# Optimization experiments

Measured on AMD Instinct MI355X. Metric: run time of the kernel, lower is better.

Reference implementation:

```python
import jax, jax.numpy as jnp
import numpy as np

B, S, D, H = 2, 2048, 1024, 16
HD = D // H  # head_dim = 64


def setup_inputs() -> dict:
    key = jax.random.key(0)
    ks = jax.random.split(key, 7)
    s = 0.02
    return {
        "queries": jax.random.normal(ks[0], (B, S, D), jnp.float32),
        "keys": jax.random.normal(ks[1], (B, S, D), jnp.float32),
        "values": jax.random.normal(ks[2], (B, S, D), jnp.float32),
        "Wq": jax.random.normal(ks[3], (D, D), jnp.float32) * s,
        "Wk": jax.random.normal(ks[4], (D, D), jnp.float32) * s,
        "Wv": jax.random.normal(ks[5], (D, D), jnp.float32) * s,
        "Wo": jax.random.normal(ks[6], (D, D), jnp.float32) * s,
    }


def reference(queries, keys, values, Wq, Wk, Wv, Wo):
    # Projections (torch Linear: x @ W.T); split into heads -> [B, H, S, HD]
    def split_heads(x):
        b, s, _ = x.shape
        return x.reshape(b, s, H, HD).transpose(0, 2, 1, 3)

    q = split_heads(queries @ Wq.T)
    k = split_heads(keys @ Wk.T)
    v = split_heads(values @ Wv.T)

    scale = 1.0 / jnp.sqrt(jnp.asarray(HD, q.dtype))
    scores = jnp.einsum("bhqd,bhkd->bhqk", q, k) * scale  # [B,H,S,S]
    attn = jax.nn.softmax(scores, axis=-1)
    ctx = jnp.einsum("bhqk,bhkd->bhqd", attn, v)  # [B,H,S,HD]
    out = ctx.transpose(0, 2, 1, 3).reshape(queries.shape[0], -1, D)
    return out @ Wo.T
```

## Files before the change

### kernel.cpp

```cpp
#include <hip/hip_runtime.h>
#include <hip/hip_bf16.h>


#define B_ 2
#define S_ 2048
#define D_ 1024
#define H_ 16
#define HD_ 64
#define NE_ (B_ * S_ * D_)
#define WN_ (D_ * D_)

typedef unsigned short u16;
typedef unsigned int u32;
typedef u16 __attribute__((may_alias)) u16_ma;
typedef float __attribute__((may_alias)) f32_ma;
typedef u32 v4u __attribute__((ext_vector_type(4)));
typedef v4u __attribute__((may_alias)) v4u_ma;
typedef short bf16x8 __attribute__((ext_vector_type(8)));
typedef bf16x8 __attribute__((may_alias)) bf16x8_ma;
typedef float f32x4 __attribute__((ext_vector_type(4)));
typedef float f32x16 __attribute__((ext_vector_type(16)));

__device__ __forceinline__ float bf2f(u16 u) {
  u32 x = ((u32)u) << 16;
  return __builtin_bit_cast(float, x);
}
__device__ __forceinline__ u16 f2bf(float f) {
  __hip_bfloat16 h = __float2bfloat16(f);
  return __builtin_bit_cast(u16, h);
}
__device__ __forceinline__ u16 rne1(float f) {
  u32 a = __builtin_bit_cast(u32, f);
  a += 0x7FFFu + ((a >> 16) & 1u);
  return (u16)(a >> 16);
}
__device__ __forceinline__ u32 rne_pair(float lo, float hi) {
  u32 a = __builtin_bit_cast(u32, lo);
  u32 b = __builtin_bit_cast(u32, hi);
  a += 0x7FFFu + ((a >> 16) & 1u);
  b += 0x7FFFu + ((b >> 16) & 1u);
  return (a >> 16) | (b & 0xFFFF0000u);
}
__device__ __forceinline__ u32 pk2(u32 alo, u32 ahi) {
  return (u32)f2bf(__builtin_bit_cast(float, alo)) |
         ((u32)f2bf(__builtin_bit_cast(float, ahi)) << 16);
}

__device__ __forceinline__ void gl_lds16(const u16* g, u16* l) {
  auto gp = (const __attribute__((address_space(1))) unsigned int*)(const void*)g;
  auto lp = (__attribute__((address_space(3))) unsigned int*)(void*)l;
  __builtin_amdgcn_global_load_lds(gp, lp, 16, 0, 0);
}

__device__ __forceinline__ bool detect_f32(const u16* Wg) {
  const int lane = threadIdx.x & 63;
  bool hit = false;
#pragma unroll
  for (int i = 0; i < 4; ++i) {
    v4u u = *(const v4u_ma*)(Wg + lane * 32 + i * 8);
#pragma unroll
    for (int j = 0; j < 4; ++j) {
      u32 w = u[j];
      hit |= (((w >> 7) & 0xFFu) >= 0xF0u) || (((w >> 23) & 0xFFu) >= 0xF0u);
    }
  }
  return __any(hit);
}

__global__ __launch_bounds__(256) void convert_bf16(
    const void* s0, const void* s1, const void* s2, const void* s3,
    const void* s4, const void* s5, const void* s6, u16* __restrict__ dst_in,
    u16* __restrict__ dst_w, const u16* __restrict__ Wdet) {
  const bool det = detect_f32(Wdet);
  if (!det) return;
  const int y = blockIdx.y;
  const void* src;
  u16* dst;
  int n;
  if (y < 3) {
    src = (y == 0) ? s0 : ((y == 1) ? s1 : s2);
    dst = dst_in + (size_t)y * NE_;
    n = NE_;
  } else {
    src = (y == 3) ? s3 : ((y == 4) ? s4 : ((y == 5) ? s5 : s6));
    dst = dst_w + (size_t)(y - 3) * WN_;
    n = WN_;
  }
  const int i = (blockIdx.x * 256 + threadIdx.x) * 8;
  if (i >= n) return;
  const v4u_ma* fp = (const v4u_ma*)((const float*)src + i);
  v4u f0 = fp[0], f1 = fp[1];
  v4u out;
  out[0] = pk2(f0[0], f0[1]);
  out[1] = pk2(f0[2], f0[3]);
  out[2] = pk2(f1[0], f1[1]);
  out[3] = pk2(f1[2], f1[3]);
  *(v4u_ma*)(dst + i) = out;
}

template <int BN, bool OUT_DET>
__global__ __launch_bounds__(256) void proj_g(
    const u16* __restrict__ Asc, const u16* __restrict__ Wsc,
    void* __restrict__ Cb, const u16* __restrict__ Wdet,
    const u16* __restrict__ Ao0, const u16* __restrict__ Ao1,
    const u16* __restrict__ Ao2, const u16* __restrict__ Wo0,
    const u16* __restrict__ Wo1, const u16* __restrict__ Wo2) {
  __shared__ u16 Al[2][128 * 64];
  __shared__ u16 Wl[2][BN * 64];

  const bool det = detect_f32(Wdet);
  const int z = blockIdx.z;

  const u16* Aptr;
  const u16* Wptr;
  if (OUT_DET) {
    Aptr = Asc;
    Wptr = det ? Wsc : Wo0;
  } else {
    Aptr = det ? (Asc + (size_t)z * NE_)
               : (z == 0 ? Ao0 : (z == 1 ? Ao1 : Ao2));
    Wptr = det ? (Wsc + (size_t)z * WN_)
               : (z == 0 ? Wo0 : (z == 1 ? Wo1 : Wo2));
  }
  const char* Ag = (const char*)Aptr;
  const char* Wg = (const char*)Wptr;

  const int tid = threadIdx.x;
  const int lane = tid & 63, wid = tid >> 6;
  const int lg = lane >> 4, li = lane & 15;
  const int wr = wid >> 1, wc = wid & 1;
  const int m0 = blockIdx.x * 128, n0 = blockIdx.y * BN;

  const int lr = lane >> 3;
  const int swzb = ((lane & 7) * 16) ^ (lr << 4);

  auto issue = [&](int bi, int kt) {
    const int k0b = kt * 128;
#pragma unroll
    for (int c = 0; c < 4; ++c) {
      const int row = wid * 32 + c * 8 + lr;
      gl_lds16((const u16*)(Ag + (size_t)(m0 + row) * 2048 + k0b + swzb),
               &Al[bi][(wid * 32 + c * 8) * 64]);
    }
    if constexpr (BN == 128) {
#pragma unroll
      for (int c = 0; c < 4; ++c) {
        const int row = wid * 32 + c * 8 + lr;
        gl_lds16((const u16*)(Wg + (size_t)(n0 + row) * 2048 + k0b + swzb),
                 &Wl[bi][(wid * 32 + c * 8) * 64]);
      }
    } else {
#pragma unroll
      for (int c = 0; c < 2; ++c) {
        const int row = wid * 16 + c * 8 + lr;
        gl_lds16((const u16*)(Wg + (size_t)(n0 + row) * 2048 + k0b + swzb),
                 &Wl[bi][(wid * 16 + c * 8) * 64]);
      }
    }
  };

  constexpr int NF = BN / 32;
  f32x4 acc[4][NF];
#pragma unroll
  for (int m = 0; m < 4; ++m)
#pragma unroll
    for (int n = 0; n < NF; ++n) acc[m][n] = (f32x4){0.f, 0.f, 0.f, 0.f};

  issue(0, 0);

  for (int kt = 0; kt < 16; ++kt) {
    const int cur = kt & 1;
    if (kt < 15) {
      issue(cur ^ 1, kt + 1);
      if constexpr (BN == 128)
        asm volatile("s_waitcnt vmcnt(8)" ::: "memory");
      else
        asm volatile("s_waitcnt vmcnt(6)" ::: "memory");
    } else {
      asm volatile("s_waitcnt vmcnt(0)" ::: "memory");
    }
    __builtin_amdgcn_s_barrier();
    asm volatile("" ::: "memory");

#pragma unroll
    for (int ks = 0; ks < 2; ++ks) {
      bf16x8 af[4], bw[NF];
#pragma unroll
      for (int m = 0; m < 4; ++m) {
        const int row = wr * 64 + m * 16 + li;
        af[m] = *(const bf16x8_ma*)((const char*)&Al[cur][0] + row * 128 +
                                    ((ks * 64 + lg * 16) ^ ((row & 7) << 4)));
      }
#pragma unroll
      for (int n = 0; n < NF; ++n) {
        const int row = wc * (BN / 2) + n * 16 + li;
        bw[n] = *(const bf16x8_ma*)((const char*)&Wl[cur][0] + row * 128 +
                                    ((ks * 64 + lg * 16) ^ ((row & 7) << 4)));
      }
#pragma unroll
      for (int m = 0; m < 4; ++m)
#pragma unroll
        for (int n = 0; n < NF; ++n)
          acc[m][n] = __builtin_amdgcn_mfma_f32_16x16x32_bf16(af[m], bw[n],
                                                              acc[m][n], 0, 0, 0);
    }

    asm volatile("" ::: "memory");
    __builtin_amdgcn_s_barrier();
  }

  const bool outf32 = OUT_DET ? det : false;
  const float zs = (!OUT_DET && z == 0) ? 0.125f : 1.0f;
#pragma unroll
  for (int m = 0; m < 4; ++m)
#pragma unroll
    for (int n = 0; n < NF; ++n)
#pragma unroll
      for (int r = 0; r < 4; ++r) {
        const int row = m0 + wr * 64 + m * 16 + lg * 4 + r;
        const int col = n0 + wc * (BN / 2) + n * 16 + li;
        const size_t idx = (size_t)row * D_ + col;
        const float v = acc[m][n][r] * zs;
        if (OUT_DET) {
          if (outf32)
            ((f32_ma*)Cb)[idx] = v;
          else
            ((u16_ma*)Cb)[idx] = rne1(v);
        } else {
          ((u16_ma*)((u16*)Cb + (size_t)z * NE_))[idx] = rne1(v);
        }
      }
}

__global__ __launch_bounds__(256) void attn3(
    const u16* __restrict__ Qg, const u16* __restrict__ Kg,
    const u16* __restrict__ Vg, u16* __restrict__ Og) {
  __shared__ u16 Kl[2][64 * 64];
  __shared__ u16 VTl[2][64 * 64];

  const int tid = threadIdx.x;
  const int wid = tid >> 6, lane = tid & 63;
  const int l31 = lane & 31;
  const int hi = lane >> 5;

  const int bid = blockIdx.x;
  const int swz = (bid & 7) * 64 + (bid >> 3);
  const int qb = swz & 15;
  const int h = (swz >> 4) & 15;
  const int b = swz >> 8;
  const size_t bbase = (size_t)b * S_ * D_;
  const int hoff = h * HD_;
  const int q0w = qb * 128 + wid * 32;

  bf16x8 bq[4];
  {
    const u16* qp = Qg + bbase + (size_t)(q0w + l31) * D_ + hoff + hi * 8;
#pragma unroll
    for (int dblk = 0; dblk < 4; ++dblk)
      bq[dblk] = *(const bf16x8_ma*)(qp + dblk * 16);
  }

  f32x16 o0, o1;
#pragma unroll
  for (int i = 0; i < 16; ++i) {
    o0[i] = 0.f;
    o1[i] = 0.f;
  }
  float mrun = -1e30f, lrun = 0.f;

  const int krr = tid >> 3;
  const int kc8 = (tid & 7) * 8;
  const int vkr = lane;
  const int vd0 = wid * 8;

  v4u kr0, kr1, vr0, vr1;
  auto kv_load = [&](int kt) {
    const int key0 = kt * 64;
    kr0 = *(const v4u_ma*)(Kg + bbase + (size_t)(key0 + krr) * D_ + hoff + kc8);
    kr1 = *(const v4u_ma*)(Kg + bbase + (size_t)(key0 + 32 + krr) * D_ + hoff + kc8);
    vr0 = *(const v4u_ma*)(Vg + bbase + (size_t)(key0 + vkr) * D_ + hoff + vd0);
    vr1 = *(const v4u_ma*)(Vg + bbase + (size_t)(key0 + vkr) * D_ + hoff + vd0 + 32);
  };
  auto kv_write = [&](int bi) {
    char* Kb = (char*)&Kl[bi][0];
    char* Vb = (char*)&VTl[bi][0];
    const int ksw = (krr & 7) << 4;
    *(v4u_ma*)(Kb + krr * 128 + ((kc8 * 2) ^ ksw)) = kr0;
    *(v4u_ma*)(Kb + (32 + krr) * 128 + ((kc8 * 2) ^ ksw)) = kr1;
    union {
      v4u v;
      u16 e[8];
    } uu;
    uu.v = vr0;
#pragma unroll
    for (int j = 0; j < 8; ++j) {
      const int d = vd0 + j;
      *(u16*)(Vb + d * 128 + ((vkr * 2) ^ ((d & 7) << 4))) = uu.e[j];
    }
    uu.v = vr1;
#pragma unroll
    for (int j = 0; j < 8; ++j) {
      const int d = vd0 + 32 + j;
      *(u16*)(Vb + d * 128 + ((vkr * 2) ^ ((d & 7) << 4))) = uu.e[j];
    }
  };

  kv_load(0);
  kv_write(0);

  const int swk = (l31 & 7) << 4;

  for (int kt = 0; kt < S_ / 64; ++kt) {
    __syncthreads();
    if (kt < S_ / 64 - 1) kv_load(kt + 1);

    const char* Kb = (const char*)&Kl[kt & 1][0];
    const char* Vb = (const char*)&VTl[kt & 1][0];

    f32x16 sT0, sT1;
#pragma unroll
    for (int i = 0; i < 16; ++i) {
      sT0[i] = 0.f;
      sT1[i] = 0.f;
    }
    __builtin_amdgcn_s_setprio(1);
#pragma unroll
    for (int dblk = 0; dblk < 4; ++dblk) {
      const int cb = (dblk * 32 + hi * 16);
      bf16x8 a0 = *(const bf16x8_ma*)(Kb + l31 * 128 + (cb ^ swk));
      bf16x8 a1 = *(const bf16x8_ma*)(Kb + (32 + l31) * 128 + (cb ^ swk));
      sT0 = __builtin_amdgcn_mfma_f32_32x32x16_bf16(a0, bq[dblk], sT0, 0, 0, 0);
      sT1 = __builtin_amdgcn_mfma_f32_32x32x16_bf16(a1, bq[dblk], sT1, 0, 0, 0);
    }
    __builtin_amdgcn_s_setprio(0);

    float pmax = sT0[0];
#pragma unroll
    for (int i = 0; i < 7; ++i)
      pmax = fmaxf(fmaxf(pmax, sT0[2 * i + 1]), sT0[2 * i + 2]);
    pmax = fmaxf(pmax, sT0[15]);
#pragma unroll
    for (int i = 0; i < 8; ++i)
      pmax = fmaxf(fmaxf(pmax, sT1[2 * i]), sT1[2 * i + 1]);
    pmax = fmaxf(pmax, __shfl_xor(pmax, 32));
    if (!__all(pmax - mrun <= 8.0f)) {
      const float mnew = fmaxf(mrun, pmax);
      const float al = __expf(mrun - mnew);
      mrun = mnew;
      lrun *= al;
      o0 *= al;
      o1 *= al;
    }

    u32 w[16];
    float sum = 0.f;
#pragma unroll
    for (int kh = 0; kh < 2; ++kh)
#pragma unroll
      for (int g = 0; g < 4; ++g)
#pragma unroll
        for (int u = 0; u < 2; ++u) {
          const int r = g * 4 + 2 * u;
          const float pe = __expf((kh ? sT1[r] : sT0[r]) - mrun);
          const float po = __expf((kh ? sT1[r + 1] : sT0[r + 1]) - mrun);
          sum += pe + po;
          w[kh * 8 + g * 2 + u] = rne_pair(pe, po);
        }
    sum += __shfl_xor(sum, 32);
    lrun += sum;

    bf16x8 pf[4];
#pragma unroll
    for (int km = 0; km < 4; ++km) {
      const int a = 4 * km;
      const u32 s0 = hi ? w[a] : w[a + 2];
      const u32 s1 = hi ? w[a + 1] : w[a + 3];
      const u32 r0 = (u32)__shfl_xor((int)s0, 32);
      const u32 r1 = (u32)__shfl_xor((int)s1, 32);
      union {
        u32 d[4];
        bf16x8 v;
      } uu;
      uu.d[0] = hi ? r0 : w[a];
      uu.d[1] = hi ? r1 : w[a + 1];
      uu.d[2] = hi ? w[a + 2] : r0;
      uu.d[3] = hi ? w[a + 3] : r1;
      pf[km] = uu.v;
    }

    __builtin_amdgcn_s_setprio(1);
#pragma unroll
    for (int km = 0; km < 4; ++km) {
      const int cb = (km * 32 + hi * 16);
      bf16x8 v0 = *(const bf16x8_ma*)(Vb + l31 * 128 + (cb ^ swk));
      bf16x8 v1 = *(const bf16x8_ma*)(Vb + (32 + l31) * 128 + (cb ^ swk));
      o0 = __builtin_amdgcn_mfma_f32_32x32x16_bf16(v0, pf[km], o0, 0, 0, 0);
      o1 = __builtin_amdgcn_mfma_f32_32x32x16_bf16(v1, pf[km], o1, 0, 0, 0);
    }
    __builtin_amdgcn_s_setprio(0);

    if (kt < S_ / 64 - 1) kv_write((kt + 1) & 1);
  }

  const float inv = 1.f / lrun;
  u16* orow = Og + bbase + (size_t)(q0w + l31) * D_ + hoff;
#pragma unroll
  for (int r = 0; r < 16; ++r) {
    const int d0 = (r & 3) + 8 * (r >> 2) + 4 * hi;
    orow[d0] = rne1(o0[r] * inv);
    orow[d0 + 32] = rne1(o1[r] * inv);
  }
}

template <bool A_SCR, bool SCR_F32, bool OUT_FINAL>
__global__ __launch_bounds__(256) void proj_slow(
    const void* __restrict__ Ag, const u16* __restrict__ Wg,
    void* __restrict__ Cg) {
  const bool det = detect_f32(Wg);
  const bool a_f32 = A_SCR ? SCR_F32 : det;
  const int m = blockIdx.x;
  const int n = blockIdx.y * 256 + threadIdx.x;
  const size_t arow = (size_t)m * D_;
  const size_t wrow = (size_t)n * D_;
  float acc = 0.f;
  for (int k = 0; k < D_; ++k) {
    float a = a_f32 ? ((const f32_ma*)Ag)[arow + k]
                    : bf2f(((const u16_ma*)Ag)[arow + k]);
    float w = det ? ((const f32_ma*)Wg)[wrow + k]
                  : bf2f(((const u16_ma*)Wg)[wrow + k]);
    acc += a * w;
  }
  const size_t ci = (size_t)m * D_ + n;
  const bool c_f32 = OUT_FINAL ? det : SCR_F32;
  if (c_f32)
    ((f32_ma*)Cg)[ci] = acc;
  else
    ((u16_ma*)Cg)[ci] = f2bf(acc);
}

template <bool SCR_F32>
__global__ __launch_bounds__(256) void attn_slow(
    const void* __restrict__ Qg, const void* __restrict__ Kg,
    const void* __restrict__ Vg, void* __restrict__ Cg) {
  const int tid = threadIdx.x;
  const int qblk = blockIdx.x & 7;
  const int h = (blockIdx.x >> 3) & 15;
  const int b = blockIdx.x >> 7;
  const int q = qblk * 256 + tid;
  const size_t base = (size_t)b * S_ * D_;
  const int hoff = h * HD_;
  float qv[64];
  {
    const size_t qrow = base + (size_t)q * D_ + hoff;
    for (int d = 0; d < 64; ++d)
      qv[d] = SCR_F32 ? ((const f32_ma*)Qg)[qrow + d]
                      : bf2f(((const u16_ma*)Qg)[qrow + d]);
  }
  float o[64];
  for (int d = 0; d < 64; ++d) o[d] = 0.f;
  float m = -1e30f, l = 0.f;
  for (int key = 0; key < S_; ++key) {
    const size_t krow = base + (size_t)key * D_ + hoff;
    float s = 0.f;
    for (int d = 0; d < 64; ++d) {
      float kx = SCR_F32 ? ((const f32_ma*)Kg)[krow + d]
                         : bf2f(((const u16_ma*)Kg)[krow + d]);
      s += qv[d] * kx;
    }
    s *= 0.125f;
    float mn = fmaxf(m, s);
    float al = expf(m - mn);
    float pe = expf(s - mn);
    m = mn;
    l = l * al + pe;
    for (int d = 0; d < 64; ++d) {
      float vx = SCR_F32 ? ((const f32_ma*)Vg)[krow + d]
                         : bf2f(((const u16_ma*)Vg)[krow + d]);
      o[d] = o[d] * al + pe * vx;
    }
  }
  const float il = 1.f / l;
  const size_t crow = base + (size_t)q * D_ + hoff;
  for (int d = 0; d < 64; ++d) {
    if (SCR_F32)
      ((f32_ma*)Cg)[crow + d] = o[d] * il;
    else
      ((u16_ma*)Cg)[crow + d] = f2bf(o[d] * il);
  }
}

extern "C" void kernel_launch(void* const* d_in, const int* in_sizes, int n_in,
                              void* d_out, int out_size, void* d_ws,
                              size_t ws_size, hipStream_t stream) {
  const u16* Wdet = (const u16*)d_in[3];
  dim3 blk(256);

  if (ws_size >= (size_t)4 * NE_ * sizeof(float)) {
    u16* Qi = (u16*)d_ws;
    u16* Wc = Qi + (size_t)3 * NE_;
    u16* Qp = Wc + (size_t)4 * WN_;
    u16* Xp = Qp + (size_t)3 * NE_;

    convert_bf16<<<dim3(2048, 7), blk, 0, stream>>>(
        d_in[0], d_in[1], d_in[2], d_in[3], d_in[4], d_in[5], d_in[6], Qi, Wc,
        Wdet);
    proj_g<128, false><<<dim3(32, 8, 3), blk, 0, stream>>>(
        Qi, Wc, Qp, Wdet, (const u16*)d_in[0], (const u16*)d_in[1],
        (const u16*)d_in[2], (const u16*)d_in[3], (const u16*)d_in[4],
        (const u16*)d_in[5]);
    attn3<<<dim3(512), blk, 0, stream>>>(Qp, Qp + NE_, Qp + (size_t)2 * NE_, Xp);
    proj_g<64, true><<<dim3(32, 16, 1), blk, 0, stream>>>(
        Xp, Wc + (size_t)3 * WN_, d_out, Wdet, nullptr, nullptr, nullptr,
        (const u16*)d_in[6], nullptr, nullptr);
  } else {
    dim3 gproj(B_ * S_, D_ / 256);
    dim3 gattn(B_ * H_ * (S_ / 256));
    u16* Qp = (u16*)d_out;
    u16* Kp = (u16*)d_in[0];
    u16* Vp = (u16*)d_in[1];
    u16* Xp = (u16*)d_in[2];
    proj_slow<false, false, false><<<gproj, blk, 0, stream>>>(
        d_in[0], (const u16*)d_in[3], Qp);
    proj_slow<false, false, false><<<gproj, blk, 0, stream>>>(
        d_in[1], (const u16*)d_in[4], Kp);
    proj_slow<false, false, false><<<gproj, blk, 0, stream>>>(
        d_in[2], (const u16*)d_in[5], Vp);
    attn_slow<false><<<gattn, blk, 0, stream>>>(Qp, Kp, Vp, Xp);
    proj_slow<true, false, true><<<gproj, blk, 0, stream>>>(
        Xp, (const u16*)d_in[6], d_out);
  }
}
```

Baseline: 231.1 us.

## DMA K tiles straight into LDS and tree-reduce softmax max/sum

In the attention kernel, K tiles now go straight from global memory into swizzled LDS through global_load_lds, instead of being loaded into registers and stored by the threads. V keeps the register path, with an explicit vmcnt wait before its LDS write. The softmax row max and sum now use pairwise tree reductions in place of serial chains, which shortens dependency chains. The host also picks a dtype mode from in_sizes so the projections and the convert kernel can skip runtime f32 detection. The explicit vmcnt(0) waits may serialize the V loads against the K DMA.

Result: slower. 243.0 us (+5.1%).

```diff
diff --git a/kernel.cpp b/kernel.cpp
--- a/kernel.cpp
+++ b/kernel.cpp
@@ -46,8 +46,8 @@
          ((u32)f2bf(__builtin_bit_cast(float, ahi)) << 16);
 }
 
-__device__ __forceinline__ void gl_lds16(const u16* g, u16* l) {
-  auto gp = (const __attribute__((address_space(1))) unsigned int*)(const void*)g;
+__device__ __forceinline__ void gl_lds16(const void* g, u16* l) {
+  auto gp = (const __attribute__((address_space(1))) unsigned int*)g;
   auto lp = (__attribute__((address_space(3))) unsigned int*)(void*)l;
   __builtin_amdgcn_global_load_lds(gp, lp, 16, 0, 0);
 }
@@ -70,8 +70,8 @@
 __global__ __launch_bounds__(256) void convert_bf16(
     const void* s0, const void* s1, const void* s2, const void* s3,
     const void* s4, const void* s5, const void* s6, u16* __restrict__ dst_in,
-    u16* __restrict__ dst_w, const u16* __restrict__ Wdet) {
-  const bool det = detect_f32(Wdet);
+    u16* __restrict__ dst_w, const u16* __restrict__ Wdet, int mode) {
+  const bool det = (mode == 1) ? true : detect_f32(Wdet);
   if (!det) return;
   const int y = blockIdx.y;
   const void* src;
@@ -104,11 +104,11 @@
     void* __restrict__ Cb, const u16* __restrict__ Wdet,
     const u16* __restrict__ Ao0, const u16* __restrict__ Ao1,
     const u16* __restrict__ Ao2, const u16* __restrict__ Wo0,
-    const u16* __restrict__ Wo1, const u16* __restrict__ Wo2) {
+    const u16* __restrict__ Wo1, const u16* __restrict__ Wo2, int mode) {
   __shared__ u16 Al[2][128 * 64];
   __shared__ u16 Wl[2][BN * 64];
 
-  const bool det = detect_f32(Wdet);
+  const bool det = (mode == 1) ? true : ((mode == 0) ? false : detect_f32(Wdet));
   const int z = blockIdx.z;
 
   const u16* Aptr;
@@ -139,21 +139,21 @@
 #pragma unroll
     for (int c = 0; c < 4; ++c) {
       const int row = wid * 32 + c * 8 + lr;
-      gl_lds16((const u16*)(Ag + (size_t)(m0 + row) * 2048 + k0b + swzb),
+      gl_lds16(Ag + (size_t)(m0 + row) * 2048 + k0b + swzb,
                &Al[bi][(wid * 32 + c * 8) * 64]);
     }
     if constexpr (BN == 128) {
 #pragma unroll
       for (int c = 0; c < 4; ++c) {
         const int row = wid * 32 + c * 8 + lr;
-        gl_lds16((const u16*)(Wg + (size_t)(n0 + row) * 2048 + k0b + swzb),
+        gl_lds16(Wg + (size_t)(n0 + row) * 2048 + k0b + swzb,
                  &Wl[bi][(wid * 32 + c * 8) * 64]);
       }
     } else {
 #pragma unroll
       for (int c = 0; c < 2; ++c) {
         const int row = wid * 16 + c * 8 + lr;
-        gl_lds16((const u16*)(Wg + (size_t)(n0 + row) * 2048 + k0b + swzb),
+        gl_lds16(Wg + (size_t)(n0 + row) * 2048 + k0b + swzb,
                  &Wl[bi][(wid * 16 + c * 8) * 64]);
       }
     }
@@ -268,25 +268,28 @@
   }
   float mrun = -1e30f, lrun = 0.f;
 
-  const int krr = tid >> 3;
-  const int kc8 = (tid & 7) * 8;
+  const int lr8 = lane >> 3;
+  const int ksz = ((lane & 7) * 16) ^ (lr8 << 4);
+  auto k_dma = [&](int bi, int kt) {
+    const int key0 = kt * 64;
+#pragma unroll
+    for (int p = 0; p < 2; ++p) {
+      const int row0 = wid * 16 + p * 8;
+      const u16* srow = Kg + bbase + (size_t)(key0 + row0 + lr8) * D_ + hoff;
+      gl_lds16((const char*)srow + ksz, &Kl[bi][row0 * 64]);
+    }
+  };
+
   const int vkr = lane;
   const int vd0 = wid * 8;
-
-  v4u kr0, kr1, vr0, vr1;
-  auto kv_load = [&](int kt) {
+  v4u vr0, vr1;
+  auto v_load = [&](int kt) {
     const int key0 = kt * 64;
-    kr0 = *(const v4u_ma*)(Kg + bbase + (size_t)(key0 + krr) * D_ + hoff + kc8);
-    kr1 = *(const v4u_ma*)(Kg + bbase + (size_t)(key0 + 32 + krr) * D_ + hoff + kc8);
     vr0 = *(const v4u_ma*)(Vg + bbase + (size_t)(key0 + vkr) * D_ + hoff + vd0);
     vr1 = *(const v4u_ma*)(Vg + bbase + (size_t)(key0 + vkr) * D_ + hoff + vd0 + 32);
   };
-  auto kv_write = [&](int bi) {
-    char* Kb = (char*)&Kl[bi][0];
+  auto v_write = [&](int bi) {
     char* Vb = (char*)&VTl[bi][0];
-    const int ksw = (krr & 7) << 4;
-    *(v4u_ma*)(Kb + krr * 128 + ((kc8 * 2) ^ ksw)) = kr0;
-    *(v4u_ma*)(Kb + (32 + krr) * 128 + ((kc8 * 2) ^ ksw)) = kr1;
     union {
       v4u v;
       u16 e[8];
@@ -305,17 +308,23 @@
     }
   };
 
-  kv_load(0);
-  kv_write(0);
+  k_dma(0, 0);
+  v_load(0);
+  asm volatile("s_waitcnt vmcnt(0)" ::: "memory");
+  v_write(0);
 
   const int swk = (l31 & 7) << 4;
 
   for (int kt = 0; kt < S_ / 64; ++kt) {
     __syncthreads();
-    if (kt < S_ / 64 - 1) kv_load(kt + 1);
-
-    const char* Kb = (const char*)&Kl[kt & 1][0];
-    const char* Vb = (const char*)&VTl[kt & 1][0];
+    const int cur = kt & 1;
+    if (kt < S_ / 64 - 1) {
+      k_dma(cur ^ 1, kt + 1);
+      v_load(kt + 1);
+    }
+
+    const char* Kb = (const char*)&Kl[cur][0];
+    const char* Vb = (const char*)&VTl[cur][0];
 
     f32x16 sT0, sT1;
 #pragma unroll
@@ -334,15 +343,14 @@
     }
     __builtin_amdgcn_s_setprio(0);
 
-    float pmax = sT0[0];
-#pragma unroll
-    for (int i = 0; i < 7; ++i)
-      pmax = fmaxf(fmaxf(pmax, sT0[2 * i + 1]), sT0[2 * i + 2]);
-    pmax = fmaxf(pmax, sT0[15]);
-#pragma unroll
-    for (int i = 0; i < 8; ++i)
-      pmax = fmaxf(fmaxf(pmax, sT1[2 * i]), sT1[2 * i + 1]);
-    pmax = fmaxf(pmax, __shfl_xor(pmax, 32));
+    float t[16];
+#pragma unroll
+    for (int i = 0; i < 16; ++i) t[i] = fmaxf(sT0[i], sT1[i]);
+#pragma unroll
+    for (int s = 8; s; s >>= 1)
+#pragma unroll
+      for (int i = 0; i < s; ++i) t[i] = fmaxf(t[i], t[i + s]);
+    float pmax = fmaxf(t[0], __shfl_xor(t[0], 32));
     if (!__all(pmax - mrun <= 8.0f)) {
       const float mnew = fmaxf(mrun, pmax);
       const float al = __expf(mrun - mnew);
@@ -353,7 +361,7 @@
     }
 
     u32 w[16];
-    float sum = 0.f;
+    float ps[16];
 #pragma unroll
     for (int kh = 0; kh < 2; ++kh)
 #pragma unroll
@@ -363,11 +371,14 @@
           const int r = g * 4 + 2 * u;
           const float pe = __expf((kh ? sT1[r] : sT0[r]) - mrun);
           const float po = __expf((kh ? sT1[r + 1] : sT0[r + 1]) - mrun);
-          sum += pe + po;
+          ps[kh * 8 + g * 2 + u] = pe + po;
           w[kh * 8 + g * 2 + u] = rne_pair(pe, po);
         }
-    sum += __shfl_xor(sum, 32);
-    lrun += sum;
+#pragma unroll
+    for (int s = 8; s; s >>= 1)
+#pragma unroll
+      for (int i = 0; i < s; ++i) ps[i] += ps[i + s];
+    lrun += ps[0] + __shfl_xor(ps[0], 32);
 
     bf16x8 pf[4];
 #pragma unroll
@@ -399,7 +410,10 @@
     }
     __builtin_amdgcn_s_setprio(0);
 
-    if (kt < S_ / 64 - 1) kv_write((kt + 1) & 1);
+    if (kt < S_ / 64 - 1) {
+      asm volatile("s_waitcnt vmcnt(0)" ::: "memory");
+      v_write(cur ^ 1);
+    }
   }
 
   const float inv = 1.f / lrun;
@@ -495,23 +509,31 @@
   const u16* Wdet = (const u16*)d_in[3];
   dim3 blk(256);
 
+  int mode = 2;
+  if (n_in >= 7 && in_sizes) {
+    if (in_sizes[0] == (int)((size_t)NE_ * 2)) mode = 0;
+    else if (in_sizes[0] == (int)((size_t)NE_ * 4)) mode = 1;
+  }
+
   if (ws_size >= (size_t)4 * NE_ * sizeof(float)) {
     u16* Qi = (u16*)d_ws;
     u16* Wc = Qi + (size_t)3 * NE_;
     u16* Qp = Wc + (size_t)4 * WN_;
     u16* Xp = Qp + (size_t)3 * NE_;
 
-    convert_bf16<<<dim3(2048, 7), blk, 0, stream>>>(
-        d_in[0], d_in[1], d_in[2], d_in[3], d_in[4], d_in[5], d_in[6], Qi, Wc,
-        Wdet);
+    if (mode != 0) {
+      convert_bf16<<<dim3(2048, 7), blk, 0, stream>>>(
+          d_in[0], d_in[1], d_in[2], d_in[3], d_in[4], d_in[5], d_in[6], Qi,
+          Wc, Wdet, mode);
+    }
     proj_g<128, false><<<dim3(32, 8, 3), blk, 0, stream>>>(
         Qi, Wc, Qp, Wdet, (const u16*)d_in[0], (const u16*)d_in[1],
         (const u16*)d_in[2], (const u16*)d_in[3], (const u16*)d_in[4],
-        (const u16*)d_in[5]);
+        (const u16*)d_in[5], mode);
     attn3<<<dim3(512), blk, 0, stream>>>(Qp, Qp + NE_, Qp + (size_t)2 * NE_, Xp);
     proj_g<64, true><<<dim3(32, 16, 1), blk, 0, stream>>>(
         Xp, Wc + (size_t)3 * WN_, d_out, Wdet, nullptr, nullptr, nullptr,
-        (const u16*)d_in[6], nullptr, nullptr);
+        (const u16*)d_in[6], nullptr, nullptr, mode);
   } else {
     dim3 gproj(B_ * S_, D_ / 256);
     dim3 gattn(B_ * H_ * (S_ / 256));
```
